# Kernel optimization log

Measured on AMD Instinct MI355X. Metric: run time of the kernel, lower is better.

Reference implementation:

```python
import jax, jax.numpy as jnp
import numpy as np

N_HEAD = 16
VEC_DIM = 1024
KV_DIM = 64
SCALE = KV_DIM ** 0.5  # q is divided by sqrt(k_v_dim)

def gelu(x):
    # torch nn.GELU default = exact erf formulation
    return jax.nn.gelu(x, approximate=False)

def setup_inputs() -> dict:
    key = jax.random.key(0)
    ks = jax.random.split(key, 12)
    B, Sq, Sk = 2, 2048, 2048
    D, H = VEC_DIM, N_HEAD * KV_DIM
    s = lambda d: 1.0 / np.sqrt(d)
    return {
        "q_vec": jax.random.normal(ks[0], (B, Sq, D), jnp.float32),
        "k_vec": jax.random.normal(ks[1], (B, Sk, D), jnp.float32),
        # weights stored [in, out] so forward is x @ W
        "wq": jax.random.normal(ks[2], (D, H), jnp.float32) * s(D),
        "wk": jax.random.normal(ks[3], (D, H), jnp.float32) * s(D),
        "wv": jax.random.normal(ks[4], (D, H), jnp.float32) * s(D),
        "w_fc1": jax.random.normal(ks[5], (H, D), jnp.float32) * s(H),
        "w_m1": jax.random.normal(ks[6], (2 * D, D), jnp.float32) * s(2 * D),
        "b_m1": jnp.zeros((D,), jnp.float32),
        "w_m2": jax.random.normal(ks[7], (D, 2 * D), jnp.float32) * s(D),
        "b_m2": jnp.zeros((2 * D,), jnp.float32),
        "w_fc2": jax.random.normal(ks[8], (2 * D, D), jnp.float32) * s(2 * D),
    }

def reference(q_vec, k_vec, wq, wk, wv, w_fc1, w_m1, b_m1, w_m2, b_m2, w_fc2):
    B, Sq, D = q_vec.shape
    Sk = k_vec.shape[1]
    # QKV projections -> [B, H, S, dh]
    q = (q_vec @ wq).reshape(B, Sq, N_HEAD, KV_DIM).transpose(0, 2, 1, 3)
    k = (k_vec @ wk).reshape(B, Sk, N_HEAD, KV_DIM).transpose(0, 2, 1, 3)
    v = (k_vec @ wv).reshape(B, Sk, N_HEAD, KV_DIM).transpose(0, 2, 1, 3)
    # naive attention: full [B,H,Sq,Sk] score matrix (faithful to source)
    scores = jnp.einsum("bhqd,bhkd->bhqk", q / SCALE, k)
    attn = jax.nn.softmax(scores, axis=-1)
    q_out = jnp.einsum("bhqk,bhkd->bhqd", attn, v)
    q_out = q_out.transpose(0, 2, 1, 3).reshape(B, Sq, N_HEAD * KV_DIM)
    q_out = gelu(q_out @ w_fc1)  # fc1 (dropout is identity at p=0)
    x = jnp.concatenate((q_vec, q_out), axis=2)  # [B, Sq, 2D]
    # MLP with residual: Linear->GELU->Linear->GELU + x
    h = gelu(gelu(x @ w_m1 + b_m1) @ w_m2 + b_m2) + x
    out = gelu(h @ w_fc2)  # fc2
    return (out, attn)
```

## Files before the change

kernel.cpp:

```cpp
#include <hip/hip_runtime.h>
#include <cstdint>


typedef _Float16 half8 __attribute__((ext_vector_type(8)));
typedef float floatx4 __attribute__((ext_vector_type(4)));

__device__ __forceinline__ floatx4 mfma16(half8 a, half8 b, floatx4 c) {
    return __builtin_amdgcn_mfma_f32_16x16x32_f16(a, b, c, 0, 0, 0);
}

__device__ __forceinline__ float gelu_f(float x) {
    return 0.5f * x * (1.0f + erff(x * 0.70710678118654752f));
}

__device__ __forceinline__ void gll16(const void* g, void* l) {
    __builtin_amdgcn_global_load_lds(
        (const __attribute__((address_space(1))) unsigned int*)g,
        (__attribute__((address_space(3))) unsigned int*)l, 16, 0, 0);
}

template <int ROWS, int GPR>
__device__ __forceinline__ void stage_gll(char* lds, const _Float16* src, int ld,
                                          int w, int l) {
    constexpr int PW = ROWS * GPR / 4;
    constexpr int NI = PW / 64;
#pragma unroll
    for (int i = 0; i < NI; i++) {
        const int idx = w * PW + i * 64 + l;
        const int r = idx / GPR;
        const int g = (idx % GPR) ^ (r & 7);
        gll16(src + (size_t)r * ld + g * 8, lds + (w * PW + i * 64) * 16);
    }
}

template <int ROWB>
__device__ __forceinline__ half8 frag(const char* lds, int row, int kbyte) {
    return *(const half8*)(lds + row * ROWB + (kbyte ^ ((row & 7) << 4)));
}


__global__ __launch_bounds__(256) void cvt_f32_f16(const float* __restrict__ src,
                                                   _Float16* __restrict__ dst, int n8) {
    int i = blockIdx.x * 256 + threadIdx.x;
    if (i < n8) {
        float4 a = ((const float4*)src)[i * 2];
        float4 b = ((const float4*)src)[i * 2 + 1];
        half8 h = {(_Float16)a.x, (_Float16)a.y, (_Float16)a.z, (_Float16)a.w,
                   (_Float16)b.x, (_Float16)b.y, (_Float16)b.z, (_Float16)b.w};
        ((half8*)dst)[i] = h;
    }
}

__global__ __launch_bounds__(256) void wtrans(const float* __restrict__ w,
                                              _Float16* __restrict__ wt, int K, int N) {
    __shared__ float tile[32][33];
    const int n0 = blockIdx.x * 32, k0 = blockIdx.y * 32;
    const int c = threadIdx.x & 31, r0 = threadIdx.x >> 5;
#pragma unroll
    for (int i = 0; i < 4; i++) {
        const int r = r0 + i * 8;
        tile[r][c] = w[(size_t)(k0 + r) * N + n0 + c];
    }
    __syncthreads();
#pragma unroll
    for (int i = 0; i < 4; i++) {
        const int r = r0 + i * 8;
        wt[(size_t)(n0 + r) * K + k0 + c] = (_Float16)tile[c][r];
    }
}


enum { E_QS = 0, E_KS = 1, E_VT = 2, E_GH = 3, E_BGH = 4, E_BGRH = 5, E_GF = 6 };

template <int EPI, bool CONCAT>
__global__ __launch_bounds__(256) void hgemm(
    int M, int N, int K,
    const _Float16* __restrict__ A, int lda, const _Float16* __restrict__ A2,
    const _Float16* __restrict__ B, int ldb,
    void* __restrict__ Cout, const float* __restrict__ bias,
    const float* __restrict__ resF, const _Float16* __restrict__ resH)
{
    __shared__ char ldsA[128 * 128];
    __shared__ char ldsB[128 * 128];
    const int t = threadIdx.x, l = t & 63, w = t >> 6;
    const int wm = w & 1, wn = w >> 1;
    const int lr = l & 15, lg = l >> 4;
    const int brow = blockIdx.y * 128, bcol = blockIdx.x * 128;

    floatx4 acc[4][4];
#pragma unroll
    for (int m = 0; m < 4; m++)
#pragma unroll
        for (int n = 0; n < 4; n++) acc[m][n] = (floatx4){0.f, 0.f, 0.f, 0.f};

    for (int k0 = 0; k0 < K; k0 += 64) {
        const _Float16* Ab = A;
        int kloc = k0;
        if constexpr (CONCAT) {
            if (k0 >= 1024) { Ab = A2; kloc = k0 - 1024; }
        }
        stage_gll<128, 8>(ldsA, Ab + (size_t)brow * lda + kloc, lda, w, l);
        stage_gll<128, 8>(ldsB, B + (size_t)bcol * ldb + k0, ldb, w, l);
        __syncthreads();
#pragma unroll
        for (int kk = 0; kk < 2; kk++) {
            const int kb = kk * 64 + lg * 16;
            half8 af[4], bf[4];
#pragma unroll
            for (int m = 0; m < 4; m++) af[m] = frag<128>(ldsA, wm * 64 + m * 16 + lr, kb);
#pragma unroll
            for (int n = 0; n < 4; n++) bf[n] = frag<128>(ldsB, wn * 64 + n * 16 + lr, kb);
#pragma unroll
            for (int m = 0; m < 4; m++)
#pragma unroll
                for (int n = 0; n < 4; n++)
                    acc[m][n] = mfma16(af[m], bf[n], acc[m][n]);
        }
        __syncthreads();
    }

#pragma unroll
    for (int m = 0; m < 4; m++)
#pragma unroll
        for (int n = 0; n < 4; n++)
#pragma unroll
            for (int r = 0; r < 4; r++) {
                const int grow = brow + wm * 64 + m * 16 + lg * 4 + r;
                const int gcol = bcol + wn * 64 + n * 16 + lr;
                float v = acc[m][n][r];
                if constexpr (EPI == E_QS) v *= 0.125f;
                if constexpr (EPI == E_QS || EPI == E_KS) {
                    const int bb = grow >> 11, s = grow & 2047;
                    const int hh = gcol >> 6, d = gcol & 63;
                    ((_Float16*)Cout)[(((size_t)(bb * 16 + hh) * 2048 + s) << 6) + d] =
                        (_Float16)v;
                } else if constexpr (EPI == E_VT) {
                    const int hh = grow >> 6, d = grow & 63;
                    const int bb = gcol >> 11, s = gcol & 2047;
                    ((_Float16*)Cout)[(((size_t)(bb * 16 + hh) * 64 + d) << 11) + s] =
                        (_Float16)v;
                } else if constexpr (EPI == E_GH) {
                    ((_Float16*)Cout)[(size_t)grow * N + gcol] = (_Float16)gelu_f(v);
                } else if constexpr (EPI == E_BGH) {
                    ((_Float16*)Cout)[(size_t)grow * N + gcol] =
                        (_Float16)gelu_f(v + bias[gcol]);
                } else if constexpr (EPI == E_BGRH) {
                    const float res = (gcol < 1024)
                        ? resF[(size_t)grow * 1024 + gcol]
                        : (float)resH[(size_t)grow * 1024 + (gcol - 1024)];
                    ((_Float16*)Cout)[(size_t)grow * N + gcol] =
                        (_Float16)(gelu_f(v + bias[gcol]) + res);
                } else {
                    ((float*)Cout)[(size_t)grow * N + gcol] = gelu_f(v);
                }
            }
}


__global__ __launch_bounds__(256) void attn_fused(
    const _Float16* __restrict__ Qh, const _Float16* __restrict__ Kh,
    const _Float16* __restrict__ Vh, float* __restrict__ attn,
    _Float16* __restrict__ QOh)
{
    __shared__ char ldsK[128 * 128];
    __shared__ char ldsV[64 * 256];
    __shared__ char ldsP[64 * 256];
    __shared__ float rsbuf[2][64];

    const int z = blockIdx.y;
    const int qs0 = blockIdx.x * 64;
    const int t = threadIdx.x, l = t & 63, w = t >> 6;
    const int wm = w & 1, wn = w >> 1;
    const int lr = l & 15, lg = l >> 4;

    const _Float16* Kz = Kh + (size_t)z * 2048 * 64;
    const _Float16* Vz = Vh + (size_t)z * 64 * 2048;

    half8 qf[2][2];
    {
        const _Float16* Qp =
            Qh + (size_t)z * 2048 * 64 + (size_t)(qs0 + wm * 32 + lr) * 64 + lg * 8;
#pragma unroll
        for (int m = 0; m < 2; m++)
#pragma unroll
            for (int kk = 0; kk < 2; kk++)
                qf[m][kk] = *(const half8*)(Qp + m * 16 * 64 + kk * 32);
    }

    float rs[2][4] = {};
    for (int it = 0; it < 16; it++) {
        stage_gll<128, 8>(ldsK, Kz + (size_t)it * 128 * 64, 64, w, l);
        __syncthreads();
        half8 kf[4][2];
#pragma unroll
        for (int n16 = 0; n16 < 4; n16++)
#pragma unroll
            for (int kk = 0; kk < 2; kk++)
                kf[n16][kk] = frag<128>(ldsK, wn * 64 + n16 * 16 + lr, kk * 64 + lg * 16);
#pragma unroll
        for (int m = 0; m < 2; m++)
#pragma unroll
            for (int n16 = 0; n16 < 4; n16++) {
                floatx4 s = {0.f, 0.f, 0.f, 0.f};
#pragma unroll
                for (int kk = 0; kk < 2; kk++) s = mfma16(qf[m][kk], kf[n16][kk], s);
#pragma unroll
                for (int r = 0; r < 4; r++) rs[m][r] += __expf(s[r]);
            }
        __syncthreads();
    }
#pragma unroll
    for (int off = 1; off < 16; off <<= 1)
#pragma unroll
        for (int m = 0; m < 2; m++)
#pragma unroll
            for (int r = 0; r < 4; r++) rs[m][r] += __shfl_xor(rs[m][r], off);
    if (lr == 0)
#pragma unroll
        for (int m = 0; m < 2; m++)
#pragma unroll
            for (int r = 0; r < 4; r++)
                rsbuf[wn][wm * 32 + m * 16 + lg * 4 + r] = rs[m][r];
    __syncthreads();
    float rinv[2][4];
#pragma unroll
    for (int m = 0; m < 2; m++)
#pragma unroll
        for (int r = 0; r < 4; r++) {
            const int row = wm * 32 + m * 16 + lg * 4 + r;
            rinv[m][r] = 1.0f / (rsbuf[0][row] + rsbuf[1][row]);
        }
    __syncthreads();

    float* attnz = attn + (size_t)z * 2048 * 2048;
    floatx4 o[2][2] = {{{0.f,0.f,0.f,0.f},{0.f,0.f,0.f,0.f}},
                       {{0.f,0.f,0.f,0.f},{0.f,0.f,0.f,0.f}}};
    for (int it = 0; it < 16; it++) {
        stage_gll<128, 8>(ldsK, Kz + (size_t)it * 128 * 64, 64, w, l);
        stage_gll<64, 16>(ldsV, Vz + it * 128, 2048, w, l);
        __syncthreads();
        half8 kf[4][2];
#pragma unroll
        for (int n16 = 0; n16 < 4; n16++)
#pragma unroll
            for (int kk = 0; kk < 2; kk++)
                kf[n16][kk] = frag<128>(ldsK, wn * 64 + n16 * 16 + lr, kk * 64 + lg * 16);
#pragma unroll
        for (int m = 0; m < 2; m++)
#pragma unroll
            for (int n16 = 0; n16 < 4; n16++) {
                floatx4 s = {0.f, 0.f, 0.f, 0.f};
#pragma unroll
                for (int kk = 0; kk < 2; kk++) s = mfma16(qf[m][kk], kf[n16][kk], s);
#pragma unroll
                for (int r = 0; r < 4; r++) {
                    const float p = __expf(s[r]) * rinv[m][r];
                    const int prow = wm * 32 + m * 16 + lg * 4 + r;
                    const int pcol = wn * 64 + n16 * 16 + lr;
                    *(_Float16*)(ldsP + prow * 256 + ((pcol * 2) ^ ((prow & 7) << 4))) =
                        (_Float16)p;
                }
            }
        __syncthreads();
#pragma unroll
        for (int i = 0; i < 4; i++) {
            const int idx = i * 256 + t;
            const int r = idx >> 4, g = idx & 15;
            half8 ph = *(const half8*)(ldsP + r * 256 + ((g * 16) ^ ((r & 7) << 4)));
            float* dst = attnz + (size_t)(qs0 + r) * 2048 + it * 128 + g * 8;
            float4 lo = {(float)ph[0], (float)ph[1], (float)ph[2], (float)ph[3]};
            float4 hi = {(float)ph[4], (float)ph[5], (float)ph[6], (float)ph[7]};
            *(float4*)dst = lo;
            *(float4*)(dst + 4) = hi;
        }
#pragma unroll
        for (int kkv = 0; kkv < 4; kkv++) {
            const int kb = kkv * 64 + lg * 16;
            half8 pf[2], vf[2];
#pragma unroll
            for (int m = 0; m < 2; m++) pf[m] = frag<256>(ldsP, wm * 32 + m * 16 + lr, kb);
#pragma unroll
            for (int n = 0; n < 2; n++) vf[n] = frag<256>(ldsV, wn * 32 + n * 16 + lr, kb);
#pragma unroll
            for (int m = 0; m < 2; m++)
#pragma unroll
                for (int n = 0; n < 2; n++) o[m][n] = mfma16(pf[m], vf[n], o[m][n]);
        }
        __syncthreads();
    }

    const int bb = z >> 4, hh = z & 15;
#pragma unroll
    for (int m = 0; m < 2; m++)
#pragma unroll
        for (int n = 0; n < 2; n++)
#pragma unroll
            for (int r = 0; r < 4; r++) {
                const int row = qs0 + wm * 32 + m * 16 + lg * 4 + r;
                const int d = wn * 32 + n * 16 + lr;
                QOh[((size_t)bb * 2048 + row) * 1024 + hh * 64 + d] = (_Float16)o[m][n][r];
            }
}


extern "C" void kernel_launch(void* const* d_in, const int* in_sizes, int n_in,
                              void* d_out, int out_size, void* d_ws, size_t ws_size,
                              hipStream_t stream)
{
    const float* q_vec = (const float*)d_in[0];
    const float* k_vec = (const float*)d_in[1];
    const float* wq    = (const float*)d_in[2];
    const float* wk    = (const float*)d_in[3];
    const float* wv    = (const float*)d_in[4];
    const float* w_fc1 = (const float*)d_in[5];
    const float* w_m1  = (const float*)d_in[6];
    const float* b_m1  = (const float*)d_in[7];
    const float* w_m2  = (const float*)d_in[8];
    const float* b_m2  = (const float*)d_in[9];
    const float* w_fc2 = (const float*)d_in[10];

    float* out  = (float*)d_out;
    float* attn = out + (size_t)2 * 2048 * 1024;

    _Float16* W = (_Float16*)d_ws;
    const size_t M1 = 1048576, M2 = 2097152, M4 = 4194304;
    _Float16* qvec_h = W;
    _Float16* kvec_h = W + M4;
    _Float16* WTq  = W + 2 * M4;
    _Float16* WTk  = WTq + M1;
    _Float16* WTv  = WTk + M1;
    _Float16* WTf1 = WTv + M1;
    _Float16* WTm1 = WTf1 + M1;
    _Float16* WTm2 = WTm1 + M2;
    _Float16* WTf2 = WTm2 + M2;
    _Float16* Qh   = WTf2 + M2;
    _Float16* Kh   = Qh + M4;
    _Float16* Vh   = Kh + M4;
    _Float16* QOh  = Vh + M4;
    _Float16* g1h  = Kh;
    _Float16* t1h  = Vh;
    _Float16* hh   = W;

    dim3 blk(256);

    cvt_f32_f16<<<dim3(2048), blk, 0, stream>>>(q_vec, qvec_h, 524288);
    cvt_f32_f16<<<dim3(2048), blk, 0, stream>>>(k_vec, kvec_h, 524288);
    wtrans<<<dim3(32, 32), blk, 0, stream>>>(wq, WTq, 1024, 1024);
    wtrans<<<dim3(32, 32), blk, 0, stream>>>(wk, WTk, 1024, 1024);
    wtrans<<<dim3(32, 32), blk, 0, stream>>>(wv, WTv, 1024, 1024);
    wtrans<<<dim3(32, 32), blk, 0, stream>>>(w_fc1, WTf1, 1024, 1024);
    wtrans<<<dim3(32, 64), blk, 0, stream>>>(w_m1, WTm1, 2048, 1024);
    wtrans<<<dim3(64, 32), blk, 0, stream>>>(w_m2, WTm2, 1024, 2048);
    wtrans<<<dim3(32, 64), blk, 0, stream>>>(w_fc2, WTf2, 2048, 1024);

    hgemm<E_QS, false><<<dim3(8, 32), blk, 0, stream>>>(
        4096, 1024, 1024, qvec_h, 1024, nullptr, WTq, 1024, Qh, nullptr, nullptr, nullptr);
    hgemm<E_KS, false><<<dim3(8, 32), blk, 0, stream>>>(
        4096, 1024, 1024, kvec_h, 1024, nullptr, WTk, 1024, Kh, nullptr, nullptr, nullptr);
    hgemm<E_VT, false><<<dim3(32, 8), blk, 0, stream>>>(
        1024, 4096, 1024, WTv, 1024, nullptr, kvec_h, 1024, Vh, nullptr, nullptr, nullptr);

    attn_fused<<<dim3(32, 32), blk, 0, stream>>>(Qh, Kh, Vh, attn, QOh);

    hgemm<E_GH, false><<<dim3(8, 32), blk, 0, stream>>>(
        4096, 1024, 1024, QOh, 1024, nullptr, WTf1, 1024, g1h, nullptr, nullptr, nullptr);
    hgemm<E_BGH, true><<<dim3(8, 32), blk, 0, stream>>>(
        4096, 1024, 2048, qvec_h, 1024, g1h, WTm1, 2048, t1h, b_m1, nullptr, nullptr);
    hgemm<E_BGRH, false><<<dim3(16, 32), blk, 0, stream>>>(
        4096, 2048, 1024, t1h, 1024, nullptr, WTm2, 1024, hh, b_m2, q_vec, g1h);
    hgemm<E_GF, false><<<dim3(8, 32), blk, 0, stream>>>(
        4096, 1024, 2048, hh, 2048, nullptr, WTf2, 2048, out, nullptr, nullptr, nullptr);
}
```

Before: 0.9999 ms.

## Double-buffer GEMM and attention tiles, merge Q/K projections, widen GEMM blocks

The GEMM kernel moves to 512-thread blocks with two LDS buffers so the next K tile is fetched while the current one is multiplied, and the Q and K projections share one launch through blockIdx.z. The attention kernel ping-pongs K tiles across buffers in the row-sum pass and prefetches the next K/V tile after loading fragments to registers in the output pass. It also writes probabilities straight to global memory from registers instead of re-reading them from LDS. The direct attention stores are narrower and less coalesced than the previous float4 path, which may hurt bandwidth on the large attention output.

```diff
diff --git a/kernel.cpp b/kernel.cpp
--- a/kernel.cpp
+++ b/kernel.cpp
@@ -19,10 +19,10 @@
         (__attribute__((address_space(3))) unsigned int*)l, 16, 0, 0);
 }
 
-template <int ROWS, int GPR>
+template <int ROWS, int GPR, int NW>
 __device__ __forceinline__ void stage_gll(char* lds, const _Float16* src, int ld,
                                           int w, int l) {
-    constexpr int PW = ROWS * GPR / 4;
+    constexpr int PW = ROWS * GPR / NW;
     constexpr int NI = PW / 64;
 #pragma unroll
     for (int i = 0; i < NI; i++) {
@@ -70,50 +70,70 @@
 }
 
 
-enum { E_QS = 0, E_KS = 1, E_VT = 2, E_GH = 3, E_BGH = 4, E_BGRH = 5, E_GF = 6 };
+enum { E_QK = 0, E_VT = 2, E_GH = 3, E_BGH = 4, E_BGRH = 5, E_GF = 6 };
 
 template <int EPI, bool CONCAT>
-__global__ __launch_bounds__(256) void hgemm(
+__global__ __launch_bounds__(512) void hgemm(
     int M, int N, int K,
-    const _Float16* __restrict__ A, int lda, const _Float16* __restrict__ A2,
-    const _Float16* __restrict__ B, int ldb,
-    void* __restrict__ Cout, const float* __restrict__ bias,
+    const _Float16* __restrict__ A, int lda, const _Float16* __restrict__ Aalt,
+    const _Float16* __restrict__ B, int ldb, const _Float16* __restrict__ Balt,
+    void* __restrict__ Cout, void* __restrict__ Coutalt,
+    const float* __restrict__ bias,
     const float* __restrict__ resF, const _Float16* __restrict__ resH)
 {
-    __shared__ char ldsA[128 * 128];
-    __shared__ char ldsB[128 * 128];
+    __shared__ char ldsA[2 * 16384];
+    __shared__ char ldsB[2 * 16384];
     const int t = threadIdx.x, l = t & 63, w = t >> 6;
     const int wm = w & 1, wn = w >> 1;
     const int lr = l & 15, lg = l >> 4;
     const int brow = blockIdx.y * 128, bcol = blockIdx.x * 128;
-
-    floatx4 acc[4][4];
-#pragma unroll
-    for (int m = 0; m < 4; m++)
-#pragma unroll
-        for (int n = 0; n < 4; n++) acc[m][n] = (floatx4){0.f, 0.f, 0.f, 0.f};
-
-    for (int k0 = 0; k0 < K; k0 += 64) {
-        const _Float16* Ab = A;
+    const int zsel = blockIdx.z;
+
+    const _Float16* Abase = A;
+    const _Float16* Bbase = B;
+    if constexpr (EPI == E_QK) {
+        if (zsel) { Abase = Aalt; Bbase = Balt; }
+    }
+
+    const int nt = K / 64;
+
+    auto stageT = [&](int tt, int buf) {
+        const int k0 = tt * 64;
+        const _Float16* Ab = Abase;
         int kloc = k0;
         if constexpr (CONCAT) {
-            if (k0 >= 1024) { Ab = A2; kloc = k0 - 1024; }
-        }
-        stage_gll<128, 8>(ldsA, Ab + (size_t)brow * lda + kloc, lda, w, l);
-        stage_gll<128, 8>(ldsB, B + (size_t)bcol * ldb + k0, ldb, w, l);
-        __syncthreads();
+            if (k0 >= 1024) { Ab = Aalt; kloc = k0 - 1024; }
+        }
+        stage_gll<128, 8, 8>(ldsA + buf * 16384, Ab + (size_t)brow * lda + kloc, lda, w, l);
+        stage_gll<128, 8, 8>(ldsB + buf * 16384, Bbase + (size_t)bcol * ldb + k0, ldb, w, l);
+    };
+
+    floatx4 acc[4][2];
+#pragma unroll
+    for (int m = 0; m < 4; m++)
+#pragma unroll
+        for (int n = 0; n < 2; n++) acc[m][n] = (floatx4){0.f, 0.f, 0.f, 0.f};
+
+    stageT(0, 0);
+    __syncthreads();
+
+    for (int tt = 0; tt < nt; ++tt) {
+        const int cur = tt & 1;
+        if (tt + 1 < nt) stageT(tt + 1, cur ^ 1);
+        const char* cA = ldsA + cur * 16384;
+        const char* cB = ldsB + cur * 16384;
 #pragma unroll
         for (int kk = 0; kk < 2; kk++) {
             const int kb = kk * 64 + lg * 16;
-            half8 af[4], bf[4];
-#pragma unroll
-            for (int m = 0; m < 4; m++) af[m] = frag<128>(ldsA, wm * 64 + m * 16 + lr, kb);
-#pragma unroll
-            for (int n = 0; n < 4; n++) bf[n] = frag<128>(ldsB, wn * 64 + n * 16 + lr, kb);
+            half8 af[4], bf[2];
+#pragma unroll
+            for (int m = 0; m < 4; m++) af[m] = frag<128>(cA, wm * 64 + m * 16 + lr, kb);
+#pragma unroll
+            for (int n = 0; n < 2; n++) bf[n] = frag<128>(cB, wn * 32 + n * 16 + lr, kb);
 #pragma unroll
             for (int m = 0; m < 4; m++)
 #pragma unroll
-                for (int n = 0; n < 4; n++)
+                for (int n = 0; n < 2; n++)
                     acc[m][n] = mfma16(af[m], bf[n], acc[m][n]);
         }
         __syncthreads();
@@ -122,18 +142,18 @@
 #pragma unroll
     for (int m = 0; m < 4; m++)
 #pragma unroll
-        for (int n = 0; n < 4; n++)
+        for (int n = 0; n < 2; n++)
 #pragma unroll
             for (int r = 0; r < 4; r++) {
                 const int grow = brow + wm * 64 + m * 16 + lg * 4 + r;
-                const int gcol = bcol + wn * 64 + n * 16 + lr;
+                const int gcol = bcol + wn * 32 + n * 16 + lr;
                 float v = acc[m][n][r];
-                if constexpr (EPI == E_QS) v *= 0.125f;
-                if constexpr (EPI == E_QS || EPI == E_KS) {
+                if constexpr (EPI == E_QK) {
                     const int bb = grow >> 11, s = grow & 2047;
                     const int hh = gcol >> 6, d = gcol & 63;
-                    ((_Float16*)Cout)[(((size_t)(bb * 16 + hh) * 2048 + s) << 6) + d] =
-                        (_Float16)v;
+                    _Float16* dst = zsel ? (_Float16*)Coutalt : (_Float16*)Cout;
+                    if (!zsel) v *= 0.125f;
+                    dst[(((size_t)(bb * 16 + hh) * 2048 + s) << 6) + d] = (_Float16)v;
                 } else if constexpr (EPI == E_VT) {
                     const int hh = grow >> 6, d = grow & 63;
                     const int bb = gcol >> 11, s = gcol & 2047;
@@ -162,9 +182,9 @@
     const _Float16* __restrict__ Vh, float* __restrict__ attn,
     _Float16* __restrict__ QOh)
 {
-    __shared__ char ldsK[128 * 128];
-    __shared__ char ldsV[64 * 256];
-    __shared__ char ldsP[64 * 256];
+    __shared__ char ldsK[16384];
+    __shared__ char ldsV[16384];
+    __shared__ char ldsP[16384];
     __shared__ float rsbuf[2][64];
 
     const int z = blockIdx.y;
@@ -188,22 +208,22 @@
     }
 
     float rs[2][4] = {};
+    stage_gll<128, 8, 4>(ldsK, Kz, 64, w, l);
+    __syncthreads();
     for (int it = 0; it < 16; it++) {
-        stage_gll<128, 8>(ldsK, Kz + (size_t)it * 128 * 64, 64, w, l);
-        __syncthreads();
-        half8 kf[4][2];
-#pragma unroll
-        for (int n16 = 0; n16 < 4; n16++)
-#pragma unroll
-            for (int kk = 0; kk < 2; kk++)
-                kf[n16][kk] = frag<128>(ldsK, wn * 64 + n16 * 16 + lr, kk * 64 + lg * 16);
+        const char* cur = (it & 1) ? ldsV : ldsK;
+        char* nxt = (it & 1) ? ldsK : ldsV;
+        if (it < 15) stage_gll<128, 8, 4>(nxt, Kz + (size_t)(it + 1) * 128 * 64, 64, w, l);
 #pragma unroll
         for (int m = 0; m < 2; m++)
 #pragma unroll
             for (int n16 = 0; n16 < 4; n16++) {
                 floatx4 s = {0.f, 0.f, 0.f, 0.f};
 #pragma unroll
-                for (int kk = 0; kk < 2; kk++) s = mfma16(qf[m][kk], kf[n16][kk], s);
+                for (int kk = 0; kk < 2; kk++)
+                    s = mfma16(qf[m][kk],
+                               frag<128>(cur, wn * 64 + n16 * 16 + lr, kk * 64 + lg * 16),
+                               s);
 #pragma unroll
                 for (int r = 0; r < 4; r++) rs[m][r] += __expf(s[r]);
             }
@@ -235,57 +255,52 @@
     float* attnz = attn + (size_t)z * 2048 * 2048;
     floatx4 o[2][2] = {{{0.f,0.f,0.f,0.f},{0.f,0.f,0.f,0.f}},
                        {{0.f,0.f,0.f,0.f},{0.f,0.f,0.f,0.f}}};
+    stage_gll<128, 8, 4>(ldsK, Kz, 64, w, l);
+    stage_gll<64, 16, 4>(ldsV, Vz, 2048, w, l);
+    __syncthreads();
     for (int it = 0; it < 16; it++) {
-        stage_gll<128, 8>(ldsK, Kz + (size_t)it * 128 * 64, 64, w, l);
-        stage_gll<64, 16>(ldsV, Vz + it * 128, 2048, w, l);
-        __syncthreads();
-        half8 kf[4][2];
-#pragma unroll
-        for (int n16 = 0; n16 < 4; n16++)
-#pragma unroll
-            for (int kk = 0; kk < 2; kk++)
-                kf[n16][kk] = frag<128>(ldsK, wn * 64 + n16 * 16 + lr, kk * 64 + lg * 16);
 #pragma unroll
         for (int m = 0; m < 2; m++)
 #pragma unroll
             for (int n16 = 0; n16 < 4; n16++) {
                 floatx4 s = {0.f, 0.f, 0.f, 0.f};
 #pragma unroll
-                for (int kk = 0; kk < 2; kk++) s = mfma16(qf[m][kk], kf[n16][kk], s);
+                for (int kk = 0; kk < 2; kk++)
+                    s = mfma16(qf[m][kk],
+                               frag<128>(ldsK, wn * 64 + n16 * 16 + lr, kk * 64 + lg * 16),
+                               s);
 #pragma unroll
                 for (int r = 0; r < 4; r++) {
                     const float p = __expf(s[r]) * rinv[m][r];
                     const int prow = wm * 32 + m * 16 + lg * 4 + r;
                     const int pcol = wn * 64 + n16 * 16 + lr;
+                    attnz[(size_t)(qs0 + prow) * 2048 + it * 128 + pcol] = p;
                     *(_Float16*)(ldsP + prow * 256 + ((pcol * 2) ^ ((prow & 7) << 4))) =
                         (_Float16)p;
                 }
             }
         __syncthreads();
-#pragma unroll
-        for (int i = 0; i < 4; i++) {
-            const int idx = i * 256 + t;
-            const int r = idx >> 4, g = idx & 15;
-            half8 ph = *(const half8*)(ldsP + r * 256 + ((g * 16) ^ ((r & 7) << 4)));
-            float* dst = attnz + (size_t)(qs0 + r) * 2048 + it * 128 + g * 8;
-            float4 lo = {(float)ph[0], (float)ph[1], (float)ph[2], (float)ph[3]};
-            float4 hi = {(float)ph[4], (float)ph[5], (float)ph[6], (float)ph[7]};
-            *(float4*)dst = lo;
-            *(float4*)(dst + 4) = hi;
-        }
+        half8 pf[2][4], vf[2][4];
 #pragma unroll
         for (int kkv = 0; kkv < 4; kkv++) {
             const int kb = kkv * 64 + lg * 16;
-            half8 pf[2], vf[2];
-#pragma unroll
-            for (int m = 0; m < 2; m++) pf[m] = frag<256>(ldsP, wm * 32 + m * 16 + lr, kb);
-#pragma unroll
-            for (int n = 0; n < 2; n++) vf[n] = frag<256>(ldsV, wn * 32 + n * 16 + lr, kb);
+#pragma unroll
+            for (int m = 0; m < 2; m++) pf[m][kkv] = frag<256>(ldsP, wm * 32 + m * 16 + lr, kb);
+#pragma unroll
+            for (int n = 0; n < 2; n++) vf[n][kkv] = frag<256>(ldsV, wn * 32 + n * 16 + lr, kb);
+        }
+        __syncthreads();
+        if (it < 15) {
+            stage_gll<128, 8, 4>(ldsK, Kz + (size_t)(it + 1) * 128 * 64, 64, w, l);
+            stage_gll<64, 16, 4>(ldsV, Vz + (it + 1) * 128, 2048, w, l);
+        }
+#pragma unroll
+        for (int kkv = 0; kkv < 4; kkv++)
 #pragma unroll
             for (int m = 0; m < 2; m++)
 #pragma unroll
-                for (int n = 0; n < 2; n++) o[m][n] = mfma16(pf[m], vf[n], o[m][n]);
-        }
+                for (int n = 0; n < 2; n++)
+                    o[m][n] = mfma16(pf[m][kkv], vf[n][kkv], o[m][n]);
         __syncthreads();
     }
 
@@ -341,7 +356,7 @@
     _Float16* t1h  = Vh;
     _Float16* hh   = W;
 
-    dim3 blk(256);
+    dim3 blk(256), blk8(512);
 
     cvt_f32_f16<<<dim3(2048), blk, 0, stream>>>(q_vec, qvec_h, 524288);
     cvt_f32_f16<<<dim3(2048), blk, 0, stream>>>(k_vec, kvec_h, 524288);
@@ -353,21 +368,25 @@
     wtrans<<<dim3(64, 32), blk, 0, stream>>>(w_m2, WTm2, 1024, 2048);
     wtrans<<<dim3(32, 64), blk, 0, stream>>>(w_fc2, WTf2, 2048, 1024);
 
-    hgemm<E_QS, false><<<dim3(8, 32), blk, 0, stream>>>(
-        4096, 1024, 1024, qvec_h, 1024, nullptr, WTq, 1024, Qh, nullptr, nullptr, nullptr);
-    hgemm<E_KS, false><<<dim3(8, 32), blk, 0, stream>>>(
-        4096, 1024, 1024, kvec_h, 1024, nullptr, WTk, 1024, Kh, nullptr, nullptr, nullptr);
-    hgemm<E_VT, false><<<dim3(32, 8), blk, 0, stream>>>(
-        1024, 4096, 1024, WTv, 1024, nullptr, kvec_h, 1024, Vh, nullptr, nullptr, nullptr);
+    hgemm<E_QK, false><<<dim3(8, 32, 2), blk8, 0, stream>>>(
+        4096, 1024, 1024, qvec_h, 1024, kvec_h, WTq, 1024, WTk,
+        Qh, Kh, nullptr, nullptr, nullptr);
+    hgemm<E_VT, false><<<dim3(32, 8, 1), blk8, 0, stream>>>(
+        1024, 4096, 1024, WTv, 1024, nullptr, kvec_h, 1024, nullptr,
+        Vh, nullptr, nullptr, nullptr, nullptr);
 
     attn_fused<<<dim3(32, 32), blk, 0, stream>>>(Qh, Kh, Vh, attn, QOh);
 
-    hgemm<E_GH, false><<<dim3(8, 32), blk, 0, stream>>>(
-        4096, 1024, 1024, QOh, 1024, nullptr, WTf1, 1024, g1h, nullptr, nullptr, nullptr);
-    hgemm<E_BGH, true><<<dim3(8, 32), blk, 0, stream>>>(
-        4096, 1024, 2048, qvec_h, 1024, g1h, WTm1, 2048, t1h, b_m1, nullptr, nullptr);
-    hgemm<E_BGRH, false><<<dim3(16, 32), blk, 0, stream>>>(
-        4096, 2048, 1024, t1h, 1024, nullptr, WTm2, 1024, hh, b_m2, q_vec, g1h);
-    hgemm<E_GF, false><<<dim3(8, 32), blk, 0, stream>>>(
-        4096, 1024, 2048, hh, 2048, nullptr, WTf2, 2048, out, nullptr, nullptr, nullptr);
-}
+    hgemm<E_GH, false><<<dim3(8, 32, 1), blk8, 0, stream>>>(
+        4096, 1024, 1024, QOh, 1024, nullptr, WTf1, 1024, nullptr,
+        g1h, nullptr, nullptr, nullptr, nullptr);
+    hgemm<E_BGH, true><<<dim3(8, 32, 1), blk8, 0, stream>>>(
+        4096, 1024, 2048, qvec_h, 1024, g1h, WTm1, 2048, nullptr,
+        t1h, nullptr, b_m1, nullptr, nullptr);
+    hgemm<E_BGRH, false><<<dim3(16, 32, 1), blk8, 0, stream>>>(
+        4096, 2048, 1024, t1h, 1024, nullptr, WTm2, 1024, nullptr,
+        hh, nullptr, b_m2, q_vec, g1h);
+    hgemm<E_GF, false><<<dim3(8, 32, 1), blk8, 0, stream>>>(
+        4096, 1024, 2048, hh, 2048, nullptr, WTf2, 2048, nullptr,
+        out, nullptr, nullptr, nullptr, nullptr);
+}
```

Result: faster. 925.8 us (-7.4%).
